# Kernel tuning notes

Hardware: AMD Instinct MI355X
Metric: run time of the kernel (lower is better)

## Reference

```python
import jax, jax.numpy as jnp
import numpy as np

TOP_K = 2
EPS = 1e-06


def setup_inputs() -> dict:
    key = jax.random.key(0)
    k1, k2 = jax.random.split(key)
    x = jax.random.normal(k1, (4, 8192, 1024), dtype=jnp.float32)
    # nn.Linear weight: [num_experts, d_model]
    W = jax.random.normal(k2, (64, 1024), dtype=jnp.float32) * (1.0 / np.sqrt(1024))
    return {"x": x, "W": W}


def reference(x, W):
    # router logits: (b, s, e)
    logits = jnp.einsum('bsd,ed->bse', x, W)
    # top-k selection (values sorted descending, like torch.topk)
    top_vals, top_idx = jax.lax.top_k(logits, TOP_K)
    top_gates = jax.nn.softmax(top_vals, axis=-1)
    # load-balance loss over full softmax probs
    probs = jax.nn.softmax(logits, axis=-1)
    avg_probs = probs.mean(axis=(0, 1))  # (e,)
    # torch.std defaults to unbiased (ddof=1)
    loss = (jnp.std(avg_probs, ddof=1) / (avg_probs.mean() + EPS)) ** 2
    return (top_idx, top_gates, loss)
```

## Files before the change

### kernel.cpp

```cpp
#include <hip/hip_runtime.h>
#include <math.h>
#include <stdint.h>


constexpr int DMODEL = 1024;
constexpr int NEXP   = 64;
constexpr int BM     = 64;
constexpr int BK     = 64;
constexpr int NTOK   = 32768;
constexpr int NTILE  = DMODEL / BK;

constexpr int LSTR = 68 * 4;
constexpr size_t WSPLIT_OFF   = 256;
constexpr size_t WSPLIT_BYTES = 384 * 1024;

typedef __attribute__((ext_vector_type(8))) short short8;
typedef __attribute__((ext_vector_type(4))) float f32x4;

__device__ __forceinline__ void gload16(const void* g, void* l) {
    __builtin_amdgcn_global_load_lds(
        (const __attribute__((address_space(1))) unsigned int*)g,
        (__attribute__((address_space(3))) unsigned int*)l,
        16, 0, 0);
}

__device__ __forceinline__ void split3(float x, short& h, short& m, short& l) {
    uint32_t u  = __float_as_uint(x);
    uint32_t uh = u & 0xffff0000u;
    float    r  = x - __uint_as_float(uh);
    uint32_t ur = __float_as_uint(r);
    uint32_t um = ur & 0xffff0000u;
    float    r2 = r - __uint_as_float(um);
    h = (short)(uh >> 16);
    m = (short)(um >> 16);
    l = (short)(__float_as_uint(r2) >> 16);
}

__global__ void wsplit_kernel(const float* __restrict__ W, char* __restrict__ dst)
{
    const int g = blockIdx.x * 256 + threadIdx.x;
    const int e = g >> 7;
    const int c = g & 127;
    const int T   = c >> 3;
    const int q   = c & 7;
    const int ks  = q >> 2;
    const int qhi = q & 3;
    const int lane = (qhi << 4) | (e & 15);
    const int nt   = e >> 4;
    const float* src = W + (size_t)e * DMODEL + c * 8;
    const float4 a = *reinterpret_cast<const float4*>(src);
    const float4 b = *reinterpret_cast<const float4*>(src + 4);
    short8 sH, sM, sL;
    const float v[8] = {a.x, a.y, a.z, a.w, b.x, b.y, b.z, b.w};
#pragma unroll
    for (int j = 0; j < 8; ++j) {
        short h, m, l; split3(v[j], h, m, l);
        sH[j] = h; sM[j] = m; sL[j] = l;
    }
    char* base = dst + ((size_t)((T * 2 + ks) * 4 + nt) * 3) * 1024
                     + (size_t)lane * 16;
    *reinterpret_cast<short8*>(base)        = sH;
    *reinterpret_cast<short8*>(base + 1024) = sM;
    *reinterpret_cast<short8*>(base + 2048) = sL;
}

__global__ __launch_bounds__(256, 2) void router_kernel(
    const float* __restrict__ x, const char* __restrict__ wsAll,
    float* __restrict__ out, float* __restrict__ expert_sums)
{
    __shared__ __align__(16) char smem[34304];

    const int tid  = threadIdx.x;
    const int lane = tid & 63;
    const int w    = tid >> 6;
    const int ks   = w & 1;
    const int nh   = w >> 1;
    const int tok0 = blockIdx.x * BM;

    f32x4 acc[4][2];
#pragma unroll
    for (int mt = 0; mt < 4; ++mt)
#pragma unroll
        for (int j = 0; j < 2; ++j) acc[mt][j] = (f32x4){0.f, 0.f, 0.f, 0.f};

    auto stageX = [&](int buf, int tile) {
#pragma unroll
        for (int i = 0; i < 4; ++i) {
            const int flat = i * 256 + tid;
            const int r = flat >> 4;
            const int c = flat & 15;
            const float* src = x + (size_t)(tok0 + r) * DMODEL + tile * BK
                                 + ((c ^ (r & 15)) << 2);
            gload16(src, smem + buf * 16384 + i * 4096 + tid * 16);
        }
    };
    auto loadW = [&](short8* bank, int tile) {
#pragma unroll
        for (int j = 0; j < 2; ++j)
#pragma unroll
            for (int cp = 0; cp < 3; ++cp) {
                const int fi = ((tile * 2 + ks) * 4 + (nh * 2 + j)) * 3 + cp;
                bank[j * 3 + cp] = *reinterpret_cast<const short8*>(
                    wsAll + (size_t)fi * 1024 + (size_t)lane * 16);
            }
    };

    short8 wb[2][6];
    stageX(0, 0);
    loadW(wb[0], 0);

#pragma unroll
    for (int t = 0; t < NTILE; ++t) {
        if (t + 1 < NTILE) {
            stageX((t + 1) & 1, t + 1);
            loadW(wb[(t + 1) & 1], t + 1);
        }
        if (t < NTILE - 1) asm volatile("s_waitcnt vmcnt(10)" ::: "memory");
        else               asm volatile("s_waitcnt vmcnt(0)"  ::: "memory");
        __builtin_amdgcn_sched_barrier(0);
        __builtin_amdgcn_s_barrier();
        __builtin_amdgcn_sched_barrier(0);

#pragma unroll
        for (int mt = 0; mt < 4; ++mt) {
            const int rl = mt * 16 + (lane & 15);
            const int c0 = ks * 8 + (lane >> 4) * 2;
            const char* xrow = smem + (t & 1) * 16384 + rl * 256;
            const float4 xa = *reinterpret_cast<const float4*>(
                xrow + ((c0 ^ (rl & 15)) << 4));
            const float4 xb = *reinterpret_cast<const float4*>(
                xrow + (((c0 + 1) ^ (rl & 15)) << 4));
            short8 aH, aM, aL;
            {
                const float v[8] = {xa.x, xa.y, xa.z, xa.w, xb.x, xb.y, xb.z, xb.w};
#pragma unroll
                for (int jj = 0; jj < 8; ++jj) {
                    short h, m, l; split3(v[jj], h, m, l);
                    aH[jj] = h; aM[jj] = m; aL[jj] = l;
                }
            }
#pragma unroll
            for (int j = 0; j < 2; ++j) {
                const short8 bH = wb[t & 1][j * 3 + 0];
                const short8 bM = wb[t & 1][j * 3 + 1];
                const short8 bL = wb[t & 1][j * 3 + 2];
                acc[mt][j] = __builtin_amdgcn_mfma_f32_16x16x32_bf16(aH, bH, acc[mt][j], 0, 0, 0);
                acc[mt][j] = __builtin_amdgcn_mfma_f32_16x16x32_bf16(aH, bM, acc[mt][j], 0, 0, 0);
                acc[mt][j] = __builtin_amdgcn_mfma_f32_16x16x32_bf16(aM, bH, acc[mt][j], 0, 0, 0);
                acc[mt][j] = __builtin_amdgcn_mfma_f32_16x16x32_bf16(aH, bL, acc[mt][j], 0, 0, 0);
                acc[mt][j] = __builtin_amdgcn_mfma_f32_16x16x32_bf16(aM, bM, acc[mt][j], 0, 0, 0);
                acc[mt][j] = __builtin_amdgcn_mfma_f32_16x16x32_bf16(aL, bH, acc[mt][j], 0, 0, 0);
            }
        }
        __builtin_amdgcn_sched_barrier(0);
        __builtin_amdgcn_s_barrier();
        __builtin_amdgcn_sched_barrier(0);
    }

    if (ks == 0) {
#pragma unroll
        for (int mt = 0; mt < 4; ++mt)
#pragma unroll
            for (int j = 0; j < 2; ++j)
#pragma unroll
                for (int r = 0; r < 4; ++r) {
                    const int tk = mt * 16 + (lane >> 4) * 4 + r;
                    const int e  = (nh * 2 + j) * 16 + (lane & 15);
                    *reinterpret_cast<float*>(smem + tk * LSTR + e * 4) = acc[mt][j][r];
                }
    }
    __syncthreads();
    if (ks == 1) {
#pragma unroll
        for (int mt = 0; mt < 4; ++mt)
#pragma unroll
            for (int j = 0; j < 2; ++j)
#pragma unroll
                for (int r = 0; r < 4; ++r) {
                    const int tk = mt * 16 + (lane >> 4) * 4 + r;
                    const int e  = (nh * 2 + j) * 16 + (lane & 15);
                    float* p = reinterpret_cast<float*>(smem + tk * LSTR + e * 4);
                    *p += acc[mt][j][r];
                }
    }
    __syncthreads();

    float* maxArr = reinterpret_cast<float*>(smem + 32768);
    float* invArr = reinterpret_cast<float*>(smem + 33024);
    float* psum   = reinterpret_cast<float*>(smem + 33280);

    if (tid < BM) {
        const char* lrow = smem + tid * LSTR;
        float4 L[16];
#pragma unroll
        for (int i = 0; i < 16; ++i)
            L[i] = *reinterpret_cast<const float4*>(lrow + i * 16);

        float mx = -INFINITY;
#pragma unroll
        for (int i = 0; i < 16; ++i)
            mx = fmaxf(mx, fmaxf(fmaxf(L[i].x, L[i].y), fmaxf(L[i].z, L[i].w)));

        float v0 = -INFINITY, v1 = -INFINITY;
        int   i0 = NEXP, i1 = NEXP;
        float s = 0.f;
#pragma unroll
        for (int i = 0; i < 16; ++i) {
            const float vv[4] = {L[i].x, L[i].y, L[i].z, L[i].w};
#pragma unroll
            for (int c = 0; c < 4; ++c) {
                const float v = vv[c];
                const int  gi = i * 4 + c;
                s += __expf(v - mx);
                if (v > v0) { v1 = v0; i1 = i0; v0 = v; i0 = gi; }
                else if (v > v1) { v1 = v; i1 = gi; }
            }
        }
        maxArr[tid] = mx;
        invArr[tid] = 1.0f / s;

        const float q = __expf(v1 - v0);
        const float d = 1.0f + q;
        const size_t tok = (size_t)tok0 + tid;
        reinterpret_cast<float2*>(out)[tok]            = make_float2((float)i0, (float)i1);
        reinterpret_cast<float2*>(out + 2 * NTOK)[tok] = make_float2(1.0f / d, q / d);
    }
    __syncthreads();

    {
        const int e = tid & 63, grp = tid >> 6;
        float s = 0.f;
#pragma unroll
        for (int i = 0; i < 16; ++i) {
            const int tk = grp * 16 + i;
            const float lg = *reinterpret_cast<const float*>(smem + tk * LSTR + e * 4);
            s += __expf(lg - maxArr[tk]) * invArr[tk];
        }
        psum[grp * 64 + e] = s;
    }
    __syncthreads();
    if (tid < 64) {
        const float s = (psum[tid] + psum[64 + tid]) + (psum[128 + tid] + psum[192 + tid]);
        atomicAdd(&expert_sums[tid], s);
    }
}

constexpr int FXS   = 0;
constexpr int FXSB  = 64 * 64 * 4;
constexpr int FWS   = 32768;
constexpr int FWSB  = 3 * 64 * 64 * 2;
constexpr int FWCMP = 64 * 64 * 2;

__global__ __launch_bounds__(512, 2) void router_fallback(
    const float* __restrict__ x, const float* __restrict__ W,
    float* __restrict__ out, float* __restrict__ expert_sums)
{
    __shared__ __align__(16) char smem[81920];

    const int tid  = threadIdx.x;
    const int lane = tid & 63;
    const int w    = tid >> 6;
    const int mt   = w & 3;
    const int kh   = w >> 2;
    const int tok0 = blockIdx.x * BM;

    f32x4 acc[4];
#pragma unroll
    for (int nt = 0; nt < 4; ++nt) acc[nt] = (f32x4){0.f, 0.f, 0.f, 0.f};

    auto stageX = [&](int buf, int tile) {
#pragma unroll
        for (int i = 0; i < 2; ++i) {
            const int r0 = w * 8 + i * 4;
            const int r  = r0 + (lane >> 4);
            const int c  = lane & 15;
            const float* src = x + (size_t)(tok0 + r) * DMODEL + tile * BK
                                 + ((c ^ (r & 15)) << 2);
            gload16(src, smem + FXS + buf * FXSB + r0 * 256 + (lane << 4));
        }
    };

    const int we  = tid >> 3;
    const int wc  = tid & 7;
    const int wph = wc ^ (we & 7);
    const float* wgp = W + (size_t)we * DMODEL + wc * 8;

    auto convW = [&](int buf, float4 a, float4 b) {
        short8 sH, sM, sL;
        float v[8] = {a.x, a.y, a.z, a.w, b.x, b.y, b.z, b.w};
#pragma unroll
        for (int j = 0; j < 8; ++j) {
            short h, m, l; split3(v[j], h, m, l);
            sH[j] = h; sM[j] = m; sL[j] = l;
        }
        char* d = smem + FWS + buf * FWSB + we * 128 + wph * 16;
        *reinterpret_cast<short8*>(d)            = sH;
        *reinterpret_cast<short8*>(d + FWCMP)    = sM;
        *reinterpret_cast<short8*>(d + 2 * FWCMP) = sL;
    };

    stageX(0, 0);
    {
        float4 a = *reinterpret_cast<const float4*>(wgp);
        float4 b = *reinterpret_cast<const float4*>(wgp + 4);
        convW(0, a, b);
    }
    __syncthreads();

    int buf = 0;
    for (int tile = 0; tile < NTILE; ++tile) {
        float4 wa, wb;
        if (tile + 1 < NTILE) {
            stageX(buf ^ 1, tile + 1);
            wa = *reinterpret_cast<const float4*>(wgp + (tile + 1) * BK);
            wb = *reinterpret_cast<const float4*>(wgp + (tile + 1) * BK + 4);
        }
        {
            const int ksl = kh;
            const int rl = mt * 16 + (lane & 15);
            const int c0 = ksl * 8 + (lane >> 4) * 2;
            const char* xrow = smem + FXS + buf * FXSB + rl * 256;
            const float4 xa = *reinterpret_cast<const float4*>(
                xrow + ((c0 ^ (rl & 15)) << 4));
            const float4 xb = *reinterpret_cast<const float4*>(
                xrow + (((c0 + 1) ^ (rl & 15)) << 4));
            short8 aH, aM, aL;
            {
                float v[8] = {xa.x, xa.y, xa.z, xa.w, xb.x, xb.y, xb.z, xb.w};
#pragma unroll
                for (int j = 0; j < 8; ++j) {
                    short h, m, l; split3(v[j], h, m, l);
                    aH[j] = h; aM[j] = m; aL[j] = l;
                }
            }
#pragma unroll
            for (int nt = 0; nt < 4; ++nt) {
                const int ef = nt * 16 + (lane & 15);
                const int q  = ksl * 4 + (lane >> 4);
                const char* wrow = smem + FWS + buf * FWSB + ef * 128
                                 + ((q ^ (ef & 7)) << 4);
                const short8 bH = *reinterpret_cast<const short8*>(wrow);
                const short8 bM = *reinterpret_cast<const short8*>(wrow + FWCMP);
                const short8 bL = *reinterpret_cast<const short8*>(wrow + 2 * FWCMP);
                acc[nt] = __builtin_amdgcn_mfma_f32_16x16x32_bf16(aH, bH, acc[nt], 0, 0, 0);
                acc[nt] = __builtin_amdgcn_mfma_f32_16x16x32_bf16(aH, bM, acc[nt], 0, 0, 0);
                acc[nt] = __builtin_amdgcn_mfma_f32_16x16x32_bf16(aM, bH, acc[nt], 0, 0, 0);
                acc[nt] = __builtin_amdgcn_mfma_f32_16x16x32_bf16(aH, bL, acc[nt], 0, 0, 0);
                acc[nt] = __builtin_amdgcn_mfma_f32_16x16x32_bf16(aM, bM, acc[nt], 0, 0, 0);
                acc[nt] = __builtin_amdgcn_mfma_f32_16x16x32_bf16(aL, bH, acc[nt], 0, 0, 0);
            }
        }
        if (tile + 1 < NTILE) convW(buf ^ 1, wa, wb);
        __syncthreads();
        buf ^= 1;
    }

    if (kh == 0) {
#pragma unroll
        for (int nt = 0; nt < 4; ++nt)
#pragma unroll
            for (int r = 0; r < 4; ++r) {
                const int t = mt * 16 + (lane >> 4) * 4 + r;
                const int e = nt * 16 + (lane & 15);
                *reinterpret_cast<float*>(smem + t * LSTR + e * 4) = acc[nt][r];
            }
    }
    __syncthreads();
    if (kh == 1) {
#pragma unroll
        for (int nt = 0; nt < 4; ++nt)
#pragma unroll
            for (int r = 0; r < 4; ++r) {
                const int t = mt * 16 + (lane >> 4) * 4 + r;
                const int e = nt * 16 + (lane & 15);
                float* p = reinterpret_cast<float*>(smem + t * LSTR + e * 4);
                *p += acc[nt][r];
            }
    }
    __syncthreads();

    float* maxArr = reinterpret_cast<float*>(smem + 18432);
    float* invArr = reinterpret_cast<float*>(smem + 18688);
    float* psum   = reinterpret_cast<float*>(smem + 18944);

    if (tid < BM) {
        const char* lrow = smem + tid * LSTR;
        float4 L[16];
#pragma unroll
        for (int i = 0; i < 16; ++i)
            L[i] = *reinterpret_cast<const float4*>(lrow + i * 16);
        float mx = -INFINITY;
#pragma unroll
        for (int i = 0; i < 16; ++i)
            mx = fmaxf(mx, fmaxf(fmaxf(L[i].x, L[i].y), fmaxf(L[i].z, L[i].w)));
        float v0 = -INFINITY, v1 = -INFINITY;
        int   i0 = NEXP, i1 = NEXP;
        float s = 0.f;
#pragma unroll
        for (int i = 0; i < 16; ++i) {
            const float vv[4] = {L[i].x, L[i].y, L[i].z, L[i].w};
#pragma unroll
            for (int c = 0; c < 4; ++c) {
                const float v = vv[c];
                const int  gi = i * 4 + c;
                s += __expf(v - mx);
                if (v > v0) { v1 = v0; i1 = i0; v0 = v; i0 = gi; }
                else if (v > v1) { v1 = v; i1 = gi; }
            }
        }
        maxArr[tid] = mx;
        invArr[tid] = 1.0f / s;
        const float q = __expf(v1 - v0);
        const float d = 1.0f + q;
        const size_t tok = (size_t)tok0 + tid;
        reinterpret_cast<float2*>(out)[tok]            = make_float2((float)i0, (float)i1);
        reinterpret_cast<float2*>(out + 2 * NTOK)[tok] = make_float2(1.0f / d, q / d);
    }
    __syncthreads();
    {
        const int e = tid & 63, grp = tid >> 6;
        float s = 0.f;
#pragma unroll
        for (int i = 0; i < 8; ++i) {
            const int t = grp * 8 + i;
            const float lg = *reinterpret_cast<const float*>(smem + t * LSTR + e * 4);
            s += __expf(lg - maxArr[t]) * invArr[t];
        }
        psum[grp * 64 + e] = s;
    }
    __syncthreads();
    if (tid < 64) {
        float s = 0.f;
#pragma unroll
        for (int g = 0; g < 8; ++g) s += psum[g * 64 + tid];
        atomicAdd(&expert_sums[tid], s);
    }
}

__global__ void loss_kernel(const float* __restrict__ sums, float* __restrict__ out)
{
    const int lane = threadIdx.x;
    float pv = sums[lane] * (1.0f / (float)NTOK);
    float m = pv;
#pragma unroll
    for (int off = 32; off; off >>= 1) m += __shfl_xor(m, off, 64);
    m *= (1.0f / (float)NEXP);
    float d = pv - m;
    float v = d * d;
#pragma unroll
    for (int off = 32; off; off >>= 1) v += __shfl_xor(v, off, 64);
    v *= (1.0f / (float)(NEXP - 1));
    if (lane == 0) {
        float stdv = sqrtf(v);
        float r = stdv / (m + 1e-6f);
        out[4 * NTOK] = r * r;
    }
}

extern "C" void kernel_launch(void* const* d_in, const int* in_sizes, int n_in,
                              void* d_out, int out_size, void* d_ws, size_t ws_size,
                              hipStream_t stream)
{
    const float* x = (const float*)d_in[0];
    const float* W = (const float*)d_in[1];
    float* out  = (float*)d_out;
    float* sums = (float*)d_ws;

    hipMemsetAsync(d_ws, 0, 256, stream);

    if (ws_size >= WSPLIT_OFF + WSPLIT_BYTES) {
        char* wsAll = (char*)d_ws + WSPLIT_OFF;
        hipLaunchKernelGGL(wsplit_kernel, dim3(32), dim3(256), 0, stream, W, wsAll);
        hipLaunchKernelGGL(router_kernel, dim3(NTOK / BM), dim3(256), 0, stream,
                           x, wsAll, out, sums);
    } else {
        hipLaunchKernelGGL(router_fallback, dim3(NTOK / BM), dim3(512), 0, stream,
                           x, W, out, sums);
    }
    hipLaunchKernelGGL(loss_kernel, dim3(1), dim3(64), 0, stream, sums, out);
}
```

Measured before the change: 55.37 us.

## Shrink router tile to 32 tokens with per-wave private X staging, no block barriers

The main router kernel now uses 32-token tiles and 128-thread blocks. Each of the two waves owns one K-half and stages its own X slice into a private LDS region, and each wave holds all 64 experts' W fragments in registers. Because no wave reads another wave's staging buffer, the per-tile block barriers are dropped and each wave waits only on its own loads (vmcnt(0)). This trades larger per-wave register use (24 short8 W buffers) and a full drain each iteration for twice as many blocks and no cross-wave synchronisation. The reduction epilogue and the fallback path are adjusted to match.

```diff
diff --git a/kernel.cpp b/kernel.cpp
--- a/kernel.cpp
+++ b/kernel.cpp
@@ -5,12 +5,13 @@
 
 constexpr int DMODEL = 1024;
 constexpr int NEXP   = 64;
-constexpr int BM     = 64;
+constexpr int BM     = 32;
 constexpr int BK     = 64;
 constexpr int NTOK   = 32768;
 constexpr int NTILE  = DMODEL / BK;
 
 constexpr int LSTR = 68 * 4;
+constexpr int LOGB = 16384;
 constexpr size_t WSPLIT_OFF   = 256;
 constexpr size_t WSPLIT_BYTES = 384 * 1024;
 
@@ -64,133 +65,126 @@
     *reinterpret_cast<short8*>(base + 2048) = sL;
 }
 
-__global__ __launch_bounds__(256, 2) void router_kernel(
+__global__ __launch_bounds__(128, 4) void router_kernel(
     const float* __restrict__ x, const char* __restrict__ wsAll,
     float* __restrict__ out, float* __restrict__ expert_sums)
 {
-    __shared__ __align__(16) char smem[34304];
+    __shared__ __align__(16) char smem[25856];
 
     const int tid  = threadIdx.x;
     const int lane = tid & 63;
     const int w    = tid >> 6;
-    const int ks   = w & 1;
-    const int nh   = w >> 1;
+    const int ks   = w;
     const int tok0 = blockIdx.x * BM;
 
-    f32x4 acc[4][2];
-#pragma unroll
-    for (int mt = 0; mt < 4; ++mt)
-#pragma unroll
-        for (int j = 0; j < 2; ++j) acc[mt][j] = (f32x4){0.f, 0.f, 0.f, 0.f};
-
-    auto stageX = [&](int buf, int tile) {
+    f32x4 acc[2][4];
+#pragma unroll
+    for (int mt = 0; mt < 2; ++mt)
+#pragma unroll
+        for (int nt = 0; nt < 4; ++nt) acc[mt][nt] = (f32x4){0.f, 0.f, 0.f, 0.f};
+
+    char* const wbase = smem + w * 8192;
+    auto stageX = [&](int buf, int t) {
 #pragma unroll
         for (int i = 0; i < 4; ++i) {
-            const int flat = i * 256 + tid;
-            const int r = flat >> 4;
-            const int c = flat & 15;
-            const float* src = x + (size_t)(tok0 + r) * DMODEL + tile * BK
-                                 + ((c ^ (r & 15)) << 2);
-            gload16(src, smem + buf * 16384 + i * 4096 + tid * 16);
+            const int r = i * 8 + (lane >> 3);
+            const int c = lane & 7;
+            const float* src = x + (size_t)(tok0 + r) * DMODEL + t * BK
+                                 + ks * 32 + ((c ^ (r & 7)) << 2);
+            gload16(src, wbase + buf * 4096 + i * 1024 + (size_t)lane * 16);
         }
     };
-    auto loadW = [&](short8* bank, int tile) {
-#pragma unroll
-        for (int j = 0; j < 2; ++j)
-#pragma unroll
-            for (int cp = 0; cp < 3; ++cp) {
-                const int fi = ((tile * 2 + ks) * 4 + (nh * 2 + j)) * 3 + cp;
-                bank[j * 3 + cp] = *reinterpret_cast<const short8*>(
-                    wsAll + (size_t)fi * 1024 + (size_t)lane * 16);
-            }
+    auto loadW = [&](short8* bank, int t) {
+        const char* wT = wsAll + (size_t)((t * 2 + ks) * 12) * 1024
+                               + (size_t)lane * 16;
+#pragma unroll
+        for (int f = 0; f < 12; ++f)
+            bank[f] = *reinterpret_cast<const short8*>(wT + f * 1024);
     };
 
-    short8 wb[2][6];
+    short8 wb[2][12];
     stageX(0, 0);
     loadW(wb[0], 0);
+    asm volatile("s_waitcnt vmcnt(0)" ::: "memory");
+    __builtin_amdgcn_sched_barrier(0);
 
 #pragma unroll
     for (int t = 0; t < NTILE; ++t) {
         if (t + 1 < NTILE) {
+            loadW(wb[(t + 1) & 1], t + 1);
             stageX((t + 1) & 1, t + 1);
-            loadW(wb[(t + 1) & 1], t + 1);
-        }
-        if (t < NTILE - 1) asm volatile("s_waitcnt vmcnt(10)" ::: "memory");
-        else               asm volatile("s_waitcnt vmcnt(0)"  ::: "memory");
-        __builtin_amdgcn_sched_barrier(0);
-        __builtin_amdgcn_s_barrier();
-        __builtin_amdgcn_sched_barrier(0);
-
-#pragma unroll
-        for (int mt = 0; mt < 4; ++mt) {
-            const int rl = mt * 16 + (lane & 15);
-            const int c0 = ks * 8 + (lane >> 4) * 2;
-            const char* xrow = smem + (t & 1) * 16384 + rl * 256;
+        }
+
+        const char* xb = wbase + (t & 1) * 4096;
+#pragma unroll
+        for (int mt = 0; mt < 2; ++mt) {
+            const int r  = mt * 16 + (lane & 15);
+            const int q0 = (lane >> 4) * 2;
+            const char* row = xb + r * 128;
             const float4 xa = *reinterpret_cast<const float4*>(
-                xrow + ((c0 ^ (rl & 15)) << 4));
-            const float4 xb = *reinterpret_cast<const float4*>(
-                xrow + (((c0 + 1) ^ (rl & 15)) << 4));
+                row + ((q0 ^ (r & 7)) << 4));
+            const float4 xc = *reinterpret_cast<const float4*>(
+                row + (((q0 + 1) ^ (r & 7)) << 4));
             short8 aH, aM, aL;
             {
-                const float v[8] = {xa.x, xa.y, xa.z, xa.w, xb.x, xb.y, xb.z, xb.w};
-#pragma unroll
-                for (int jj = 0; jj < 8; ++jj) {
-                    short h, m, l; split3(v[jj], h, m, l);
-                    aH[jj] = h; aM[jj] = m; aL[jj] = l;
+                const float v[8] = {xa.x, xa.y, xa.z, xa.w, xc.x, xc.y, xc.z, xc.w};
+#pragma unroll
+                for (int j = 0; j < 8; ++j) {
+                    short h, m, l; split3(v[j], h, m, l);
+                    aH[j] = h; aM[j] = m; aL[j] = l;
                 }
             }
 #pragma unroll
-            for (int j = 0; j < 2; ++j) {
-                const short8 bH = wb[t & 1][j * 3 + 0];
-                const short8 bM = wb[t & 1][j * 3 + 1];
-                const short8 bL = wb[t & 1][j * 3 + 2];
-                acc[mt][j] = __builtin_amdgcn_mfma_f32_16x16x32_bf16(aH, bH, acc[mt][j], 0, 0, 0);
-                acc[mt][j] = __builtin_amdgcn_mfma_f32_16x16x32_bf16(aH, bM, acc[mt][j], 0, 0, 0);
-                acc[mt][j] = __builtin_amdgcn_mfma_f32_16x16x32_bf16(aM, bH, acc[mt][j], 0, 0, 0);
-                acc[mt][j] = __builtin_amdgcn_mfma_f32_16x16x32_bf16(aH, bL, acc[mt][j], 0, 0, 0);
-                acc[mt][j] = __builtin_amdgcn_mfma_f32_16x16x32_bf16(aM, bM, acc[mt][j], 0, 0, 0);
-                acc[mt][j] = __builtin_amdgcn_mfma_f32_16x16x32_bf16(aL, bH, acc[mt][j], 0, 0, 0);
-            }
-        }
+            for (int nt = 0; nt < 4; ++nt) {
+                const short8 bH = wb[t & 1][nt * 3 + 0];
+                const short8 bM = wb[t & 1][nt * 3 + 1];
+                const short8 bL = wb[t & 1][nt * 3 + 2];
+                acc[mt][nt] = __builtin_amdgcn_mfma_f32_16x16x32_bf16(aH, bH, acc[mt][nt], 0, 0, 0);
+                acc[mt][nt] = __builtin_amdgcn_mfma_f32_16x16x32_bf16(aH, bM, acc[mt][nt], 0, 0, 0);
+                acc[mt][nt] = __builtin_amdgcn_mfma_f32_16x16x32_bf16(aM, bH, acc[mt][nt], 0, 0, 0);
+                acc[mt][nt] = __builtin_amdgcn_mfma_f32_16x16x32_bf16(aH, bL, acc[mt][nt], 0, 0, 0);
+                acc[mt][nt] = __builtin_amdgcn_mfma_f32_16x16x32_bf16(aM, bM, acc[mt][nt], 0, 0, 0);
+                acc[mt][nt] = __builtin_amdgcn_mfma_f32_16x16x32_bf16(aL, bH, acc[mt][nt], 0, 0, 0);
+            }
+        }
+        asm volatile("s_waitcnt vmcnt(0)" ::: "memory");
         __builtin_amdgcn_sched_barrier(0);
-        __builtin_amdgcn_s_barrier();
-        __builtin_amdgcn_sched_barrier(0);
-    }
-
-    if (ks == 0) {
-#pragma unroll
-        for (int mt = 0; mt < 4; ++mt)
-#pragma unroll
-            for (int j = 0; j < 2; ++j)
+    }
+
+    if (w == 0) {
+#pragma unroll
+        for (int mt = 0; mt < 2; ++mt)
+#pragma unroll
+            for (int nt = 0; nt < 4; ++nt)
 #pragma unroll
                 for (int r = 0; r < 4; ++r) {
                     const int tk = mt * 16 + (lane >> 4) * 4 + r;
-                    const int e  = (nh * 2 + j) * 16 + (lane & 15);
-                    *reinterpret_cast<float*>(smem + tk * LSTR + e * 4) = acc[mt][j][r];
+                    const int e  = nt * 16 + (lane & 15);
+                    *reinterpret_cast<float*>(smem + LOGB + tk * LSTR + e * 4) = acc[mt][nt][r];
                 }
     }
     __syncthreads();
-    if (ks == 1) {
-#pragma unroll
-        for (int mt = 0; mt < 4; ++mt)
-#pragma unroll
-            for (int j = 0; j < 2; ++j)
+    if (w == 1) {
+#pragma unroll
+        for (int mt = 0; mt < 2; ++mt)
+#pragma unroll
+            for (int nt = 0; nt < 4; ++nt)
 #pragma unroll
                 for (int r = 0; r < 4; ++r) {
                     const int tk = mt * 16 + (lane >> 4) * 4 + r;
-                    const int e  = (nh * 2 + j) * 16 + (lane & 15);
-                    float* p = reinterpret_cast<float*>(smem + tk * LSTR + e * 4);
-                    *p += acc[mt][j][r];
+                    const int e  = nt * 16 + (lane & 15);
+                    float* p = reinterpret_cast<float*>(smem + LOGB + tk * LSTR + e * 4);
+                    *p += acc[mt][nt][r];
                 }
     }
     __syncthreads();
 
-    float* maxArr = reinterpret_cast<float*>(smem + 32768);
-    float* invArr = reinterpret_cast<float*>(smem + 33024);
-    float* psum   = reinterpret_cast<float*>(smem + 33280);
+    float* maxArr = reinterpret_cast<float*>(smem + 25088);
+    float* invArr = reinterpret_cast<float*>(smem + 25216);
+    float* psum   = reinterpret_cast<float*>(smem + 25344);
 
     if (tid < BM) {
-        const char* lrow = smem + tid * LSTR;
+        const char* lrow = smem + LOGB + tid * LSTR;
         float4 L[16];
 #pragma unroll
         for (int i = 0; i < 16; ++i)
@@ -233,18 +227,18 @@
 #pragma unroll
         for (int i = 0; i < 16; ++i) {
             const int tk = grp * 16 + i;
-            const float lg = *reinterpret_cast<const float*>(smem + tk * LSTR + e * 4);
+            const float lg = *reinterpret_cast<const float*>(smem + LOGB + tk * LSTR + e * 4);
             s += __expf(lg - maxArr[tk]) * invArr[tk];
         }
         psum[grp * 64 + e] = s;
     }
     __syncthreads();
     if (tid < 64) {
-        const float s = (psum[tid] + psum[64 + tid]) + (psum[128 + tid] + psum[192 + tid]);
-        atomicAdd(&expert_sums[tid], s);
-    }
-}
-
+        atomicAdd(&expert_sums[tid], psum[tid] + psum[64 + tid]);
+    }
+}
+
+constexpr int FBM   = 64;
 constexpr int FXS   = 0;
 constexpr int FXSB  = 64 * 64 * 4;
 constexpr int FWS   = 32768;
@@ -262,7 +256,7 @@
     const int w    = tid >> 6;
     const int mt   = w & 3;
     const int kh   = w >> 2;
-    const int tok0 = blockIdx.x * BM;
+    const int tok0 = blockIdx.x * FBM;
 
     f32x4 acc[4];
 #pragma unroll
@@ -294,8 +288,8 @@
             sH[j] = h; sM[j] = m; sL[j] = l;
         }
         char* d = smem + FWS + buf * FWSB + we * 128 + wph * 16;
-        *reinterpret_cast<short8*>(d)            = sH;
-        *reinterpret_cast<short8*>(d + FWCMP)    = sM;
+        *reinterpret_cast<short8*>(d)             = sH;
+        *reinterpret_cast<short8*>(d + FWCMP)     = sM;
         *reinterpret_cast<short8*>(d + 2 * FWCMP) = sL;
     };
 
@@ -322,11 +316,11 @@
             const char* xrow = smem + FXS + buf * FXSB + rl * 256;
             const float4 xa = *reinterpret_cast<const float4*>(
                 xrow + ((c0 ^ (rl & 15)) << 4));
-            const float4 xb = *reinterpret_cast<const float4*>(
+            const float4 xc = *reinterpret_cast<const float4*>(
                 xrow + (((c0 + 1) ^ (rl & 15)) << 4));
             short8 aH, aM, aL;
             {
-                float v[8] = {xa.x, xa.y, xa.z, xa.w, xb.x, xb.y, xb.z, xb.w};
+                float v[8] = {xa.x, xa.y, xa.z, xa.w, xc.x, xc.y, xc.z, xc.w};
 #pragma unroll
                 for (int j = 0; j < 8; ++j) {
                     short h, m, l; split3(v[j], h, m, l);
@@ -383,7 +377,7 @@
     float* invArr = reinterpret_cast<float*>(smem + 18688);
     float* psum   = reinterpret_cast<float*>(smem + 18944);
 
-    if (tid < BM) {
+    if (tid < FBM) {
         const char* lrow = smem + tid * LSTR;
         float4 L[16];
 #pragma unroll
@@ -471,10 +465,10 @@
     if (ws_size >= WSPLIT_OFF + WSPLIT_BYTES) {
         char* wsAll = (char*)d_ws + WSPLIT_OFF;
         hipLaunchKernelGGL(wsplit_kernel, dim3(32), dim3(256), 0, stream, W, wsAll);
-        hipLaunchKernelGGL(router_kernel, dim3(NTOK / BM), dim3(256), 0, stream,
+        hipLaunchKernelGGL(router_kernel, dim3(NTOK / BM), dim3(128), 0, stream,
                            x, wsAll, out, sums);
     } else {
-        hipLaunchKernelGGL(router_fallback, dim3(NTOK / BM), dim3(512), 0, stream,
+        hipLaunchKernelGGL(router_fallback, dim3(NTOK / FBM), dim3(512), 0, stream,
                            x, W, out, sums);
     }
     hipLaunchKernelGGL(loss_kernel, dim3(1), dim3(64), 0, stream, sums, out);
```

Measured after the change: 64.97 us. 1.17x slower.

## Triple-buffer x tiles in LDS with one barrier per k-step

Applied to the files above, without the earlier changes.

Moves the X staging from double to triple buffering in LDS, prefetching two tiles ahead, and issues loads after the barrier so only one barrier per iteration is needed. W register prefetch stays double-buffered but is issued after the barrier. Launch bounds are raised to three blocks per CU to match the larger LDS footprint. The goal is deeper memory latency hiding and less synchronisation, at the cost of more LDS and possible register pressure under the tighter occupancy bound.

```diff
diff --git a/kernel.cpp b/kernel.cpp
--- a/kernel.cpp
+++ b/kernel.cpp
@@ -11,6 +11,7 @@
 constexpr int NTILE  = DMODEL / BK;
 
 constexpr int LSTR = 68 * 4;
+constexpr int XBUF = 16384;
 constexpr size_t WSPLIT_OFF   = 256;
 constexpr size_t WSPLIT_BYTES = 384 * 1024;
 
@@ -64,11 +65,11 @@
     *reinterpret_cast<short8*>(base + 2048) = sL;
 }
 
-__global__ __launch_bounds__(256, 2) void router_kernel(
+__global__ __launch_bounds__(256, 3) void router_kernel(
     const float* __restrict__ x, const char* __restrict__ wsAll,
     float* __restrict__ out, float* __restrict__ expert_sums)
 {
-    __shared__ __align__(16) char smem[34304];
+    __shared__ __align__(16) char smem[50688];
 
     const int tid  = threadIdx.x;
     const int lane = tid & 63;
@@ -83,56 +84,59 @@
 #pragma unroll
         for (int j = 0; j < 2; ++j) acc[mt][j] = (f32x4){0.f, 0.f, 0.f, 0.f};
 
-    auto stageX = [&](int buf, int tile) {
+    auto stageX = [&](int buf, int t) {
 #pragma unroll
         for (int i = 0; i < 4; ++i) {
             const int flat = i * 256 + tid;
             const int r = flat >> 4;
             const int c = flat & 15;
-            const float* src = x + (size_t)(tok0 + r) * DMODEL + tile * BK
+            const float* src = x + (size_t)(tok0 + r) * DMODEL + t * BK
                                  + ((c ^ (r & 15)) << 2);
-            gload16(src, smem + buf * 16384 + i * 4096 + tid * 16);
+            gload16(src, smem + buf * XBUF + flat * 16);
         }
     };
-    auto loadW = [&](short8* bank, int tile) {
+    auto loadW = [&](short8* bank, int t) {
+        const char* wT = wsAll + (size_t)lane * 16;
 #pragma unroll
         for (int j = 0; j < 2; ++j)
 #pragma unroll
             for (int cp = 0; cp < 3; ++cp) {
-                const int fi = ((tile * 2 + ks) * 4 + (nh * 2 + j)) * 3 + cp;
+                const int fi = ((t * 2 + ks) * 4 + (nh * 2 + j)) * 3 + cp;
                 bank[j * 3 + cp] = *reinterpret_cast<const short8*>(
-                    wsAll + (size_t)fi * 1024 + (size_t)lane * 16);
+                    wT + (size_t)fi * 1024);
             }
     };
 
-    short8 wb[2][6];
+    short8 wb0[6], wb1[6];
     stageX(0, 0);
-    loadW(wb[0], 0);
+    loadW(wb0, 0);
+    stageX(1, 1);
 
 #pragma unroll
     for (int t = 0; t < NTILE; ++t) {
-        if (t + 1 < NTILE) {
-            stageX((t + 1) & 1, t + 1);
-            loadW(wb[(t + 1) & 1], t + 1);
-        }
-        if (t < NTILE - 1) asm volatile("s_waitcnt vmcnt(10)" ::: "memory");
-        else               asm volatile("s_waitcnt vmcnt(0)"  ::: "memory");
+        if (t == NTILE - 1) asm volatile("s_waitcnt vmcnt(0)" ::: "memory");
+        else                asm volatile("s_waitcnt vmcnt(4)" ::: "memory");
         __builtin_amdgcn_sched_barrier(0);
         __builtin_amdgcn_s_barrier();
         __builtin_amdgcn_sched_barrier(0);
 
+        if (t + 1 < NTILE) loadW((t & 1) ? wb0 : wb1, t + 1);
+        if (t + 2 < NTILE) stageX((t + 2) % 3, t + 2);
+
+        const char* xb = smem + (t % 3) * XBUF;
+        const short8* wbank = (t & 1) ? wb1 : wb0;
 #pragma unroll
         for (int mt = 0; mt < 4; ++mt) {
             const int rl = mt * 16 + (lane & 15);
             const int c0 = ks * 8 + (lane >> 4) * 2;
-            const char* xrow = smem + (t & 1) * 16384 + rl * 256;
+            const char* xrow = xb + rl * 256;
             const float4 xa = *reinterpret_cast<const float4*>(
                 xrow + ((c0 ^ (rl & 15)) << 4));
-            const float4 xb = *reinterpret_cast<const float4*>(
+            const float4 xc = *reinterpret_cast<const float4*>(
                 xrow + (((c0 + 1) ^ (rl & 15)) << 4));
             short8 aH, aM, aL;
             {
-                const float v[8] = {xa.x, xa.y, xa.z, xa.w, xb.x, xb.y, xb.z, xb.w};
+                const float v[8] = {xa.x, xa.y, xa.z, xa.w, xc.x, xc.y, xc.z, xc.w};
 #pragma unroll
                 for (int jj = 0; jj < 8; ++jj) {
                     short h, m, l; split3(v[jj], h, m, l);
@@ -141,9 +145,9 @@
             }
 #pragma unroll
             for (int j = 0; j < 2; ++j) {
-                const short8 bH = wb[t & 1][j * 3 + 0];
-                const short8 bM = wb[t & 1][j * 3 + 1];
-                const short8 bL = wb[t & 1][j * 3 + 2];
+                const short8 bH = wbank[j * 3 + 0];
+                const short8 bM = wbank[j * 3 + 1];
+                const short8 bL = wbank[j * 3 + 2];
                 acc[mt][j] = __builtin_amdgcn_mfma_f32_16x16x32_bf16(aH, bH, acc[mt][j], 0, 0, 0);
                 acc[mt][j] = __builtin_amdgcn_mfma_f32_16x16x32_bf16(aH, bM, acc[mt][j], 0, 0, 0);
                 acc[mt][j] = __builtin_amdgcn_mfma_f32_16x16x32_bf16(aM, bH, acc[mt][j], 0, 0, 0);
@@ -152,10 +156,8 @@
                 acc[mt][j] = __builtin_amdgcn_mfma_f32_16x16x32_bf16(aL, bH, acc[mt][j], 0, 0, 0);
             }
         }
-        __builtin_amdgcn_sched_barrier(0);
-        __builtin_amdgcn_s_barrier();
-        __builtin_amdgcn_sched_barrier(0);
-    }
+    }
+    __syncthreads();
 
     if (ks == 0) {
 #pragma unroll
@@ -185,9 +187,9 @@
     }
     __syncthreads();
 
-    float* maxArr = reinterpret_cast<float*>(smem + 32768);
-    float* invArr = reinterpret_cast<float*>(smem + 33024);
-    float* psum   = reinterpret_cast<float*>(smem + 33280);
+    float* maxArr = reinterpret_cast<float*>(smem + 49152);
+    float* invArr = reinterpret_cast<float*>(smem + 49408);
+    float* psum   = reinterpret_cast<float*>(smem + 49664);
 
     if (tid < BM) {
         const char* lrow = smem + tid * LSTR;
@@ -245,6 +247,7 @@
     }
 }
 
+constexpr int FBM   = 64;
 constexpr int FXS   = 0;
 constexpr int FXSB  = 64 * 64 * 4;
 constexpr int FWS   = 32768;
@@ -262,7 +265,7 @@
     const int w    = tid >> 6;
     const int mt   = w & 3;
     const int kh   = w >> 2;
-    const int tok0 = blockIdx.x * BM;
+    const int tok0 = blockIdx.x * FBM;
 
     f32x4 acc[4];
 #pragma unroll
@@ -294,8 +297,8 @@
             sH[j] = h; sM[j] = m; sL[j] = l;
         }
         char* d = smem + FWS + buf * FWSB + we * 128 + wph * 16;
-        *reinterpret_cast<short8*>(d)            = sH;
-        *reinterpret_cast<short8*>(d + FWCMP)    = sM;
+        *reinterpret_cast<short8*>(d)             = sH;
+        *reinterpret_cast<short8*>(d + FWCMP)     = sM;
         *reinterpret_cast<short8*>(d + 2 * FWCMP) = sL;
     };
 
@@ -322,11 +325,11 @@
             const char* xrow = smem + FXS + buf * FXSB + rl * 256;
             const float4 xa = *reinterpret_cast<const float4*>(
                 xrow + ((c0 ^ (rl & 15)) << 4));
-            const float4 xb = *reinterpret_cast<const float4*>(
+            const float4 xc = *reinterpret_cast<const float4*>(
                 xrow + (((c0 + 1) ^ (rl & 15)) << 4));
             short8 aH, aM, aL;
             {
-                float v[8] = {xa.x, xa.y, xa.z, xa.w, xb.x, xb.y, xb.z, xb.w};
+                float v[8] = {xa.x, xa.y, xa.z, xa.w, xc.x, xc.y, xc.z, xc.w};
 #pragma unroll
                 for (int j = 0; j < 8; ++j) {
                     short h, m, l; split3(v[j], h, m, l);
@@ -383,7 +386,7 @@
     float* invArr = reinterpret_cast<float*>(smem + 18688);
     float* psum   = reinterpret_cast<float*>(smem + 18944);
 
-    if (tid < BM) {
+    if (tid < FBM) {
         const char* lrow = smem + tid * LSTR;
         float4 L[16];
 #pragma unroll
@@ -474,7 +477,7 @@
         hipLaunchKernelGGL(router_kernel, dim3(NTOK / BM), dim3(256), 0, stream,
                            x, wsAll, out, sums);
     } else {
-        hipLaunchKernelGGL(router_fallback, dim3(NTOK / BM), dim3(512), 0, stream,
+        hipLaunchKernelGGL(router_fallback, dim3(NTOK / FBM), dim3(512), 0, stream,
                            x, W, out, sums);
     }
     hipLaunchKernelGGL(loss_kernel, dim3(1), dim3(64), 0, stream, sums, out);
```

Result: slower. 58.93 us (+6.4%).
